# Optimization experiments

Measured on AMD Instinct MI355X. Metric: run time of the kernel, lower is better.

## Reference

```python
import jax, jax.numpy as jnp
import numpy as np

B, S, D, H, HD, TOPK = 2, 2048, 2048, 16, 128, 256
HIDDEN = 4 * D
EPS = 1e-6


def setup_inputs() -> dict:
    key = jax.random.key(0)
    ks = jax.random.split(key, 12)
    def g(k, shape, scale):
        return jax.random.normal(k, shape, dtype=jnp.float32) * scale
    # rotary tables: freqs_cis[s, i] = (cos, sin) of s * theta_i
    theta = 1.0 / (10000.0 ** (np.arange(0, HD, 2, dtype=np.float32) / HD))  # [HD/2]
    ang = np.arange(S, dtype=np.float32)[:, None] * theta[None, :]           # [S, HD/2]
    freqs_cis = jnp.asarray(np.stack([np.cos(ang), np.sin(ang)], axis=-1))   # [S, HD/2, 2]
    return {
        "x": g(ks[0], (B, S, D), 1.0),
        "start_pos": 0,
        "freqs_cis": freqs_cis,
        "router_w": g(ks[1], (D, 1), D ** -0.5),
        "wq": g(ks[2], (D, H * HD), D ** -0.5),
        "wk": g(ks[3], (D, H * HD), D ** -0.5),
        "wv": g(ks[4], (D, H * HD), D ** -0.5),
        "wo": g(ks[5], (H * HD, D), (H * HD) ** -0.5),
        "w1": g(ks[6], (D, HIDDEN), D ** -0.5),
        "w2": g(ks[7], (HIDDEN, D), HIDDEN ** -0.5),
        "w3": g(ks[8], (D, HIDDEN), D ** -0.5),
        "attn_norm_w": jnp.ones((D,), jnp.float32),
        "ffn_norm_w": jnp.ones((D,), jnp.float32),
    }


def _rmsnorm(x, w, eps=EPS):
    return x * jax.lax.rsqrt(jnp.mean(x * x, axis=-1, keepdims=True) + eps) * w


def _rotary(q, freqs):  # q: [B,S,H,HD], freqs: [S,HD/2,2]
    q = q.reshape(*q.shape[:-1], HD // 2, 2)
    cos = freqs[None, :, None, :, 0]
    sin = freqs[None, :, None, :, 1]
    qr = q[..., 0] * cos - q[..., 1] * sin
    qi = q[..., 0] * sin + q[..., 1] * cos
    return jnp.stack([qr, qi], axis=-1).reshape(*q.shape[:-2], HD)


def _attention(xn, freqs, tok_mask, wq, wk, wv, wo):
    b, s, _ = xn.shape
    q = (xn @ wq).reshape(b, s, H, HD)
    k = (xn @ wk).reshape(b, s, H, HD)
    v = (xn @ wv).reshape(b, s, H, HD)
    q = _rotary(q, freqs)
    k = _rotary(k, freqs)
    scores = jnp.einsum("bqhd,bkhd->bhqk", q, k) / np.sqrt(HD).astype(np.float32)
    # keys of non-selected tokens are masked out (MoD routing mask)
    scores = scores + jnp.where(tok_mask[:, None, None, :] > 0, 0.0, -1e9)
    attn = jax.nn.softmax(scores, axis=-1)
    out = jnp.einsum("bhqk,bkhd->bqhd", attn, v).reshape(b, s, H * HD)
    return out @ wo


def reference(x, start_pos, freqs_cis, router_w, wq, wk, wv, wo, w1, w2, w3, attn_norm_w, ffn_norm_w):
    b, s, _ = x.shape
    freqs = jax.lax.dynamic_slice_in_dim(freqs_cis, start_pos, s, axis=0)
    # --- router: top-k token selection + scatter mask ---
    token_weights = x @ router_w                      # [B,S,1]
    topk_vals, topk_idx = jax.lax.top_k(token_weights[..., 0], TOPK)
    mask = jnp.zeros((b, s), x.dtype).at[jnp.arange(b)[:, None], topk_idx].set(1.0)
    masked_input = x * mask[:, :, None]
    # --- dense attention + FFN on masked tokens ---
    h = masked_input + _attention(_rmsnorm(masked_input, attn_norm_w), freqs, mask, wq, wk, wv, wo)
    hn = _rmsnorm(h, ffn_norm_w)
    out = (jax.nn.silu(hn @ w1) * (hn @ w3)) @ w2    # SwiGLU FFN
    return out, token_weights, topk_idx
```

## Files before the change

kernel.cpp:

```cpp
#include <hip/hip_runtime.h>
#include <hip/hip_bf16.h>
#include <math.h>

#define B_ 2
#define S_ 2048
#define D_ 2048
#define H_ 16
#define HD_ 128
#define TOPK_ 256
#define HIDDEN_ 8192
#define EPS_ 1e-6f

constexpr int ROWS_SEL = B_ * TOPK_;
constexpr int ROWS_ALL = ROWS_SEL + B_;

typedef __attribute__((ext_vector_type(8))) short bf16x8;
typedef __attribute__((ext_vector_type(4))) float f32x4;

__device__ __forceinline__ short f2bf(float f) {
    __hip_bfloat16 h = __float2bfloat16(f);
    return *reinterpret_cast<short*>(&h);
}

__device__ __forceinline__ float bf2f(short s) {
    union { unsigned u; float f; } c;
    c.u = ((unsigned)(unsigned short)s) << 16;
    return c.f;
}

__device__ __forceinline__ void gll16(const void* g, void* l) {
    __builtin_amdgcn_global_load_lds(
        (const __attribute__((address_space(1))) unsigned int*)g,
        (__attribute__((address_space(3))) unsigned int*)l, 16, 0, 0);
}

__device__ __forceinline__ float block_sum_256(float v, float* red4) {
    for (int o = 32; o; o >>= 1) v += __shfl_down(v, o);
    if ((threadIdx.x & 63) == 0) red4[threadIdx.x >> 6] = v;
    __syncthreads();
    float t = red4[0] + red4[1] + red4[2] + red4[3];
    __syncthreads();
    return t;
}

__device__ __forceinline__ float block_max_256(float v, float* red4) {
    for (int o = 32; o; o >>= 1) v = fmaxf(v, __shfl_down(v, o));
    if ((threadIdx.x & 63) == 0) red4[threadIdx.x >> 6] = v;
    __syncthreads();
    float t = fmaxf(fmaxf(red4[0], red4[1]), fmaxf(red4[2], red4[3]));
    __syncthreads();
    return t;
}

__global__ __launch_bounds__(256) void router_kernel(const float* __restrict__ x,
                                                     const float* __restrict__ rw,
                                                     float* __restrict__ tw) {
    int token = blockIdx.x;
    const float4* xr = (const float4*)(x + (long)token * D_);
    const float4* r4 = (const float4*)rw;
    float s = 0.f;
    for (int c = threadIdx.x; c < D_ / 4; c += 256) {
        float4 a = xr[c], b = r4[c];
        s += a.x * b.x + a.y * b.y + a.z * b.z + a.w * b.w;
    }
    __shared__ float red4[4];
    float tot = block_sum_256(s, red4);
    if (threadIdx.x == 0) tw[token] = tot;
}

__global__ __launch_bounds__(1024) void topk_kernel(const float* __restrict__ tw,
                                                    float* __restrict__ idx_out,
                                                    int* __restrict__ sel_idx,
                                                    int* __restrict__ sel_pos) {
    int b = blockIdx.x;
    __shared__ float v[S_];
    __shared__ int id[S_];
    int t = threadIdx.x;
    for (int i = t; i < S_; i += 1024) {
        v[i] = tw[b * S_ + i];
        id[i] = i;
        sel_pos[b * S_ + i] = -1;
    }
    __syncthreads();
    for (int k = 2; k <= S_; k <<= 1) {
        for (int j = k >> 1; j > 0; j >>= 1) {
            for (int i = t; i < S_; i += 1024) {
                int ixj = i ^ j;
                if (ixj > i) {
                    float va = v[i], vb = v[ixj];
                    int ia = id[i], ib = id[ixj];
                    bool before = (va > vb) || (va == vb && ia < ib);
                    bool dir = ((i & k) == 0);
                    if (dir != before) {
                        v[i] = vb; v[ixj] = va;
                        id[i] = ib; id[ixj] = ia;
                    }
                }
            }
            __syncthreads();
        }
    }
    if (t < TOPK_) {
        idx_out[b * TOPK_ + t] = (float)id[t];
        sel_idx[b * TOPK_ + t] = id[t];
        sel_pos[b * S_ + id[t]] = t;
    }
}

__global__ __launch_bounds__(256) void gather_rmsnorm_kernel(const float* __restrict__ x,
                                                             const int* __restrict__ sel_idx,
                                                             const float* __restrict__ nw,
                                                             short* __restrict__ XN) {
    int r = blockIdx.x;
    int b = r >> 8;
    int s = sel_idx[r];
    const float* xr = x + ((long)b * S_ + s) * D_;
    __shared__ float buf[D_];
    __shared__ float red4[4];
    float ss = 0.f;
    for (int c = threadIdx.x; c < D_; c += 256) {
        float vv = xr[c];
        buf[c] = vv;
        ss += vv * vv;
    }
    float tot = block_sum_256(ss, red4);
    float scale = rsqrtf(tot / D_ + EPS_);
    for (int c = threadIdx.x; c < D_; c += 256)
        XN[(long)r * D_ + c] = f2bf(buf[c] * scale * nw[c]);
}

__global__ __launch_bounds__(256) void gemm_mfma_w(
    const short* __restrict__ A,
    const float* __restrict__ B0, const float* __restrict__ B1, const float* __restrict__ B2,
    float* __restrict__ Cb, long czStride, long spStride,
    int M, int N, int Ktot, int K_per, int splits) {
    __shared__ short As[128 * 32];
    __shared__ float Bs[32 * 128];
    int z = blockIdx.z;
    int zmat = z / splits, sp = z % splits;
    const float* Bm = (zmat == 0) ? B0 : (zmat == 1) ? B1 : B2;
    float* C = Cb + (long)zmat * czStride + (long)sp * spStride;
    int kbase = sp * K_per;
    int row0 = blockIdx.y * 128, col0 = blockIdx.x * 128;
    int t = threadIdx.x;
    int lane = t & 63, w = t >> 6;
    int l16 = lane & 15, quad = lane >> 4;
    int wr = (w >> 1) * 64, wc = (w & 1) * 64;
    int arr = t >> 2, ach = (t & 3) * 8;
    int bkr = t >> 5, bnc = (t & 31) * 4;
    f32x4 acc[4][4] = {};
    for (int k0 = kbase; k0 < kbase + K_per; k0 += 32) {
        __syncthreads();
        #pragma unroll
        for (int rd = 0; rd < 2; ++rd) {
            int ar = row0 + arr + rd * 64; ar = (ar < M) ? ar : (M - 1);
            gll16(A + (size_t)ar * Ktot + k0 + ach, (char*)As + rd * 4096 + t * 16);
        }
        #pragma unroll
        for (int rd = 0; rd < 4; ++rd) {
            int kr = k0 + rd * 8 + bkr;
            gll16(Bm + (size_t)kr * N + col0 + bnc, (char*)Bs + rd * 4096 + t * 16);
        }
        __syncthreads();
        bf16x8 af[4], bf[4];
        #pragma unroll
        for (int i = 0; i < 4; ++i)
            af[i] = *(const bf16x8*)(As + (wr + i * 16 + l16) * 32 + quad * 8);
        #pragma unroll
        for (int j = 0; j < 4; ++j) {
            int n = wc + j * 16 + l16;
            union { short s[8]; bf16x8 v; } ub;
            #pragma unroll
            for (int jj = 0; jj < 8; ++jj)
                ub.s[jj] = f2bf(Bs[(quad * 8 + jj) * 128 + n]);
            bf[j] = ub.v;
        }
        #pragma unroll
        for (int i = 0; i < 4; ++i)
            #pragma unroll
            for (int j = 0; j < 4; ++j)
                acc[i][j] = __builtin_amdgcn_mfma_f32_16x16x32_bf16(af[i], bf[j], acc[i][j], 0, 0, 0);
    }
    #pragma unroll
    for (int i = 0; i < 4; ++i) {
        #pragma unroll
        for (int r = 0; r < 4; ++r) {
            int row = row0 + wr + i * 16 + quad * 4 + r;
            if (row < M) {
                #pragma unroll
                for (int j = 0; j < 4; ++j)
                    C[(size_t)row * N + col0 + wc + j * 16 + l16] = acc[i][j][r];
            }
        }
    }
}

template <bool OBF>
__global__ __launch_bounds__(256) void gemm_mfma_attn(
    const short* __restrict__ A, long sAo, long sAi, int lda,
    const short* __restrict__ Bm, long sBo, long sBi, int ldb,
    void* __restrict__ Cv, long sCo, long sCi, int ldc,
    int M, int N, int K, int inner) {
    __shared__ short smem[2 * 128 * 32];
    short* As = smem;
    short* Bs = smem + 128 * 32;
    int z = blockIdx.z;
    int zo = z / inner, zi = z % inner;
    const short* Ab = A + (long)zo * sAo + (long)zi * sAi;
    const short* Bb = Bm + (long)zo * sBo + (long)zi * sBi;
    long cbase = (long)zo * sCo + (long)zi * sCi;
    int row0 = blockIdx.y * 128, col0 = blockIdx.x * 128;
    int t = threadIdx.x;
    int lane = t & 63, w = t >> 6;
    int l16 = lane & 15, quad = lane >> 4;
    int wr = (w >> 1) * 64, wc = (w & 1) * 64;
    int rr = t >> 2, ch = (t & 3) * 8;
    f32x4 acc[4][4] = {};
    for (int k0 = 0; k0 < K; k0 += 32) {
        __syncthreads();
        #pragma unroll
        for (int rd = 0; rd < 2; ++rd) {
            int r = rr + rd * 64;
            int ar = row0 + r; ar = (ar < M) ? ar : (M - 1);
            gll16(Ab + (size_t)ar * lda + k0 + ch, (char*)As + rd * 4096 + t * 16);
            gll16(Bb + (size_t)(col0 + r) * ldb + k0 + ch, (char*)Bs + rd * 4096 + t * 16);
        }
        __syncthreads();
        bf16x8 af[4], bfr[4];
        #pragma unroll
        for (int i = 0; i < 4; ++i)
            af[i] = *(const bf16x8*)(As + (wr + i * 16 + l16) * 32 + quad * 8);
        #pragma unroll
        for (int j = 0; j < 4; ++j)
            bfr[j] = *(const bf16x8*)(Bs + (wc + j * 16 + l16) * 32 + quad * 8);
        #pragma unroll
        for (int i = 0; i < 4; ++i)
            #pragma unroll
            for (int j = 0; j < 4; ++j)
                acc[i][j] = __builtin_amdgcn_mfma_f32_16x16x32_bf16(af[i], bfr[j], acc[i][j], 0, 0, 0);
    }
    #pragma unroll
    for (int i = 0; i < 4; ++i) {
        #pragma unroll
        for (int r = 0; r < 4; ++r) {
            int row = row0 + wr + i * 16 + quad * 4 + r;
            if (row < M) {
                #pragma unroll
                for (int j = 0; j < 4; ++j) {
                    long idx = cbase + (size_t)row * ldc + col0 + wc + j * 16 + l16;
                    if (OBF) ((short*)Cv)[idx] = f2bf(acc[i][j][r]);
                    else     ((float*)Cv)[idx] = acc[i][j][r];
                }
            }
        }
    }
}

__global__ __launch_bounds__(256) void qkv_finish(
    const float* __restrict__ Cp, const float* __restrict__ fc,
    const int* __restrict__ sel_idx, const int* __restrict__ sp0,
    short* __restrict__ Qbf, short* __restrict__ Kbf, short* __restrict__ Vbf,
    int splits) {
    int r = blockIdx.x;
    int s = sel_idx[r];
    int pos = sp0[0] + s;
    const float* f = fc + (long)pos * HD_;
    const long matS = (long)ROWS_SEL * D_;
    const long spS = 3 * matS;
    const float* qp = Cp + (long)r * D_;
    const float* kp = qp + matS;
    const float* vp = qp + 2 * matS;
    const float qscale = 0.08838834764831845f;
    for (int p = threadIdx.x; p < (D_ / 2); p += 256) {
        int h = p >> 6, d2 = p & 63;
        int e0 = h * HD_ + d2 * 2;
        float q0 = 0.f, q1 = 0.f, k0 = 0.f, k1 = 0.f, v0 = 0.f, v1 = 0.f;
        for (int sp = 0; sp < splits; ++sp) {
            long off = (long)sp * spS;
            q0 += qp[off + e0]; q1 += qp[off + e0 + 1];
            k0 += kp[off + e0]; k1 += kp[off + e0 + 1];
            v0 += vp[off + e0]; v1 += vp[off + e0 + 1];
        }
        float c = f[d2 * 2], sn = f[d2 * 2 + 1];
        Qbf[(long)r * D_ + e0]     = f2bf((q0 * c - q1 * sn) * qscale);
        Qbf[(long)r * D_ + e0 + 1] = f2bf((q0 * sn + q1 * c) * qscale);
        Kbf[(long)r * D_ + e0]     = f2bf(k0 * c - k1 * sn);
        Kbf[(long)r * D_ + e0 + 1] = f2bf(k0 * sn + k1 * c);
        Vbf[(long)r * D_ + e0]     = f2bf(v0);
        Vbf[(long)r * D_ + e0 + 1] = f2bf(v1);
    }
}

__global__ __launch_bounds__(256) void vt_kernel(const short* __restrict__ Vbf,
                                                 short* __restrict__ VT) {
    int z = blockIdx.z;
    int b = z >> 4, h = z & 15;
    int key0 = blockIdx.x * 64, d0 = blockIdx.y * 64;
    __shared__ short L[64][72];
    int t = threadIdx.x;
    int kr = t >> 3, dc = (t & 7) * 8;
    #pragma unroll
    for (int rr = 0; rr < 2; ++rr) {
        int key = kr + rr * 32;
        union { short s[8]; int4 v; } u;
        u.v = *(const int4*)&Vbf[(size_t)(b * 256 + key0 + key) * D_ + h * 128 + d0 + dc];
        #pragma unroll
        for (int j = 0; j < 8; ++j) L[key][dc + j] = u.s[j];
    }
    __syncthreads();
    int dr = t >> 3, kc = (t & 7) * 8;
    #pragma unroll
    for (int rr = 0; rr < 2; ++rr) {
        int d = dr + rr * 32;
        union { short s[8]; int4 v; } u;
        #pragma unroll
        for (int j = 0; j < 8; ++j) u.s[j] = L[kc + j][d];
        *(int4*)&VT[((size_t)z * 128 + d0 + d) * 256 + key0 + kc] = u.v;
    }
}

__global__ __launch_bounds__(256) void softmax_kernel(const float* __restrict__ SC,
                                                      short* __restrict__ Pbf) {
    long row = blockIdx.x;
    const float* p = SC + row * 256;
    int t = threadIdx.x;
    float v = p[t];
    __shared__ float red4[4];
    float m = block_max_256(v, red4);
    float e = expf(v - m);
    float s = block_sum_256(e, red4);
    Pbf[row * 256 + t] = f2bf(e / s);
}

__global__ __launch_bounds__(256) void vbar_kernel(const short* __restrict__ Vbf,
                                                   short* __restrict__ Obf) {
    int b = blockIdx.y;
    int c = blockIdx.x * 256 + threadIdx.x;
    float s = 0.f;
    for (int i = 0; i < TOPK_; ++i) s += bf2f(Vbf[((long)b * TOPK_ + i) * D_ + c]);
    Obf[(long)(ROWS_SEL + b) * D_ + c] = f2bf(s * (1.f / TOPK_));
}

__global__ __launch_bounds__(256) void resid_rmsnorm_kernel(const float* __restrict__ Pp,
                                                            int splits,
                                                            const float* __restrict__ x,
                                                            const int* __restrict__ sel_idx,
                                                            const float* __restrict__ nw,
                                                            short* __restrict__ HN) {
    int r = blockIdx.x;
    __shared__ float buf[D_];
    __shared__ float red4[4];
    const long spS = (long)ROWS_ALL * D_;
    const float* pr = Pp + (long)r * D_;
    const float* xr = nullptr;
    if (r < ROWS_SEL) {
        int b = r >> 8;
        int s = sel_idx[r];
        xr = x + ((long)b * S_ + s) * D_;
    }
    float ss = 0.f;
    for (int c = threadIdx.x; c < D_; c += 256) {
        float v = xr ? xr[c] : 0.f;
        for (int sp = 0; sp < splits; ++sp) v += pr[(long)sp * spS + c];
        buf[c] = v;
        ss += v * v;
    }
    float tot = block_sum_256(ss, red4);
    float scale = rsqrtf(tot / D_ + EPS_);
    for (int c = threadIdx.x; c < D_; c += 256)
        HN[(long)r * D_ + c] = f2bf(buf[c] * scale * nw[c]);
}

__global__ __launch_bounds__(256) void reduce_silu_kernel(const float* __restrict__ Gp,
                                                          short* __restrict__ FF, long n) {
    long i = (long)blockIdx.x * 256 + threadIdx.x;
    if (i < n) {
        const long cz = (long)ROWS_ALL * HIDDEN_;
        float a = Gp[i] + Gp[cz + i];
        float g = Gp[2 * cz + i] + Gp[3 * cz + i];
        FF[i] = f2bf((a / (1.f + expf(-a))) * g);
    }
}

__global__ __launch_bounds__(256) void w2_reduce_kernel(const float* __restrict__ Wp,
                                                        float* __restrict__ OUTR, long n4) {
    long i = (long)blockIdx.x * 256 + threadIdx.x;
    if (i < n4) {
        const long spS4 = (long)ROWS_ALL * D_ / 4;
        float4 s = ((const float4*)Wp)[i];
        for (int sp = 1; sp < 8; ++sp) {
            float4 v = ((const float4*)Wp)[(long)sp * spS4 + i];
            s.x += v.x; s.y += v.y; s.z += v.z; s.w += v.w;
        }
        ((float4*)OUTR)[i] = s;
    }
}

__global__ __launch_bounds__(256) void scatter_kernel(const float* __restrict__ OUTR,
                                                      const int* __restrict__ sel_pos,
                                                      float* __restrict__ out) {
    int blk = blockIdx.x;
    int b = blk >> 11;
    int p = sel_pos[blk];
    int row = (p >= 0) ? (b * TOPK_ + p) : (ROWS_SEL + b);
    const float4* src = (const float4*)(OUTR + (long)row * D_);
    float4* dst = (float4*)(out + (long)blk * D_);
    for (int c = threadIdx.x; c < D_ / 4; c += 256) dst[c] = src[c];
}

extern "C" void kernel_launch(void* const* d_in, const int* in_sizes, int n_in,
                              void* d_out, int out_size, void* d_ws, size_t ws_size,
                              hipStream_t stream) {
    const float* x        = (const float*)d_in[0];
    const int*   startpos = (const int*)d_in[1];
    const float* freqs    = (const float*)d_in[2];
    const float* router_w = (const float*)d_in[3];
    const float* wq       = (const float*)d_in[4];
    const float* wk       = (const float*)d_in[5];
    const float* wv       = (const float*)d_in[6];
    const float* wo       = (const float*)d_in[7];
    const float* w1       = (const float*)d_in[8];
    const float* w2       = (const float*)d_in[9];
    const float* w3       = (const float*)d_in[10];
    const float* attn_w   = (const float*)d_in[11];
    const float* ffn_w    = (const float*)d_in[12];

    float* out     = (float*)d_out;
    float* tw_out  = out + (long)B_ * S_ * D_;
    float* idx_out = tw_out + (long)B_ * S_;

    char* ws = (char*)d_ws;
    auto alloc = [&](size_t bytes) -> void* {
        void* p = (void*)ws;
        ws += (bytes + 255) / 256 * 256;
        return p;
    };
    int*   sel_idx = (int*)alloc((size_t)B_ * TOPK_ * sizeof(int));
    int*   sel_pos = (int*)alloc((size_t)B_ * S_ * sizeof(int));
    short* XNbf = (short*)alloc((size_t)ROWS_SEL * D_ * sizeof(short));
    short* Qbf  = (short*)alloc((size_t)ROWS_SEL * D_ * sizeof(short));
    short* Kbf  = (short*)alloc((size_t)ROWS_SEL * D_ * sizeof(short));
    short* Vbf  = (short*)alloc((size_t)ROWS_SEL * D_ * sizeof(short));
    short* VT   = (short*)alloc((size_t)B_ * H_ * HD_ * TOPK_ * sizeof(short));
    float* SC   = (float*)alloc((size_t)B_ * H_ * TOPK_ * TOPK_ * sizeof(float));
    short* Pbf  = (short*)alloc((size_t)B_ * H_ * TOPK_ * TOPK_ * sizeof(short));
    short* Obf  = (short*)alloc((size_t)ROWS_ALL * D_ * sizeof(short));
    short* HNbf = (short*)alloc((size_t)ROWS_ALL * D_ * sizeof(short));
    short* FFbf = (short*)alloc((size_t)ROWS_ALL * HIDDEN_ * sizeof(short));
    float* OUTR = (float*)alloc((size_t)ROWS_ALL * D_ * sizeof(float));
    float* Gar  = (float*)alloc((size_t)4 * ROWS_ALL * HIDDEN_ * sizeof(float));

    router_kernel<<<B_ * S_, 256, 0, stream>>>(x, router_w, tw_out);
    topk_kernel<<<B_, 1024, 0, stream>>>(tw_out, idx_out, sel_idx, sel_pos);
    gather_rmsnorm_kernel<<<ROWS_SEL, 256, 0, stream>>>(x, sel_idx, attn_w, XNbf);
    {
        dim3 g(D_ / 128, ROWS_SEL / 128, 3 * 4);
        gemm_mfma_w<<<g, 256, 0, stream>>>(XNbf, wq, wk, wv,
                                           Gar, (long)ROWS_SEL * D_, (long)3 * ROWS_SEL * D_,
                                           ROWS_SEL, D_, D_, D_ / 4, 4);
    }
    qkv_finish<<<ROWS_SEL, 256, 0, stream>>>(Gar, freqs, sel_idx, startpos, Qbf, Kbf, Vbf, 4);
    {
        dim3 g(4, 2, B_ * H_);
        vt_kernel<<<g, 256, 0, stream>>>(Vbf, VT);
    }
    {
        dim3 g(2, 2, B_ * H_);
        gemm_mfma_attn<false><<<g, 256, 0, stream>>>(
            Qbf, (long)TOPK_ * D_, HD_, D_,
            Kbf, (long)TOPK_ * D_, HD_, D_,
            SC, (long)H_ * TOPK_ * TOPK_, (long)TOPK_ * TOPK_, TOPK_,
            TOPK_, TOPK_, HD_, H_);
    }
    softmax_kernel<<<B_ * H_ * TOPK_, 256, 0, stream>>>(SC, Pbf);
    {
        dim3 g(1, 2, B_ * H_);
        gemm_mfma_attn<true><<<g, 256, 0, stream>>>(
            Pbf, (long)H_ * TOPK_ * TOPK_, (long)TOPK_ * TOPK_, TOPK_,
            VT, (long)H_ * HD_ * TOPK_, (long)HD_ * TOPK_, TOPK_,
            Obf, (long)TOPK_ * D_, HD_, D_,
            TOPK_, HD_, TOPK_, H_);
    }
    {
        dim3 g(D_ / 256, B_, 1);
        vbar_kernel<<<g, 256, 0, stream>>>(Vbf, Obf);
    }
    {
        dim3 g(D_ / 128, (ROWS_ALL + 127) / 128, 8);
        gemm_mfma_w<<<g, 256, 0, stream>>>(Obf, wo, wo, wo,
                                           Gar, 0, (long)ROWS_ALL * D_,
                                           ROWS_ALL, D_, D_, D_ / 8, 8);
    }
    resid_rmsnorm_kernel<<<ROWS_ALL, 256, 0, stream>>>(Gar, 8, x, sel_idx, ffn_w, HNbf);
    {
        dim3 g(HIDDEN_ / 128, (ROWS_ALL + 127) / 128, 2 * 2);
        gemm_mfma_w<<<g, 256, 0, stream>>>(HNbf, w1, w3, w3,
                                           Gar, (long)2 * ROWS_ALL * HIDDEN_, (long)ROWS_ALL * HIDDEN_,
                                           ROWS_ALL, HIDDEN_, D_, D_ / 2, 2);
    }
    {
        long n = (long)ROWS_ALL * HIDDEN_;
        reduce_silu_kernel<<<(unsigned)((n + 255) / 256), 256, 0, stream>>>(Gar, FFbf, n);
    }
    {
        dim3 g(D_ / 128, (ROWS_ALL + 127) / 128, 8);
        gemm_mfma_w<<<g, 256, 0, stream>>>(FFbf, w2, w2, w2,
                                           Gar, 0, (long)ROWS_ALL * D_,
                                           ROWS_ALL, D_, HIDDEN_, HIDDEN_ / 8, 8);
    }
    {
        long n4 = (long)ROWS_ALL * D_ / 4;
        w2_reduce_kernel<<<(unsigned)((n4 + 255) / 256), 256, 0, stream>>>(Gar, OUTR, n4);
    }
    scatter_kernel<<<B_ * S_, 256, 0, stream>>>(OUTR, sel_pos, out);
}
```

Before: 570.8 us.

## Pre-transpose weights to bf16 K-major and load B fragments directly

Adds a per-call kernel that converts each fp32 weight matrix to bf16 and transposes it to N×K layout through shared memory. The GEMM can then stage B tiles with the same 16-byte direct loads as A and read MFMA fragments as contiguous bf16x8 vectors. This removes the strided per-element fp32 LDS reads and bf16 conversions from the inner loop and halves LDS use for B. In exchange, every call makes an extra full pass over all weights: roughly 256MB read and 128MB written, plus extra workspace.

```diff
diff --git a/kernel.cpp b/kernel.cpp
--- a/kernel.cpp
+++ b/kernel.cpp
@@ -50,6 +50,34 @@
     float t = fmaxf(fmaxf(red4[0], red4[1]), fmaxf(red4[2], red4[3]));
     __syncthreads();
     return t;
+}
+
+__global__ __launch_bounds__(256) void wtrans_kernel(const float* __restrict__ Wsrc,
+                                                     short* __restrict__ WT,
+                                                     int K, int N) {
+    int k0 = blockIdx.y * 64, n0 = blockIdx.x * 64;
+    __shared__ short L[64][72];
+    int t = threadIdx.x;
+    int r = t >> 4, c4 = (t & 15) * 4;
+    #pragma unroll
+    for (int p = 0; p < 4; ++p) {
+        int kr = r + p * 16;
+        float4 v = *(const float4*)&Wsrc[(size_t)(k0 + kr) * N + n0 + c4];
+        L[kr][c4 + 0] = f2bf(v.x);
+        L[kr][c4 + 1] = f2bf(v.y);
+        L[kr][c4 + 2] = f2bf(v.z);
+        L[kr][c4 + 3] = f2bf(v.w);
+    }
+    __syncthreads();
+    int dr = t >> 3, kc = (t & 7) * 8;
+    #pragma unroll
+    for (int p = 0; p < 2; ++p) {
+        int n = dr + p * 32;
+        union { short s[8]; int4 v; } u;
+        #pragma unroll
+        for (int j = 0; j < 8; ++j) u.s[j] = L[kc + j][n];
+        *(int4*)&WT[(size_t)(n0 + n) * K + k0 + kc] = u.v;
+    }
 }
 
 __global__ __launch_bounds__(256) void router_kernel(const float* __restrict__ x,
@@ -129,16 +157,17 @@
         XN[(long)r * D_ + c] = f2bf(buf[c] * scale * nw[c]);
 }
 
-__global__ __launch_bounds__(256) void gemm_mfma_w(
+__global__ __launch_bounds__(256) void gemm_mfma_wbt(
     const short* __restrict__ A,
-    const float* __restrict__ B0, const float* __restrict__ B1, const float* __restrict__ B2,
+    const short* __restrict__ T0, const short* __restrict__ T1, const short* __restrict__ T2,
     float* __restrict__ Cb, long czStride, long spStride,
     int M, int N, int Ktot, int K_per, int splits) {
-    __shared__ short As[128 * 32];
-    __shared__ float Bs[32 * 128];
+    __shared__ short smem[2 * 128 * 32];
+    short* As = smem;
+    short* Bs = smem + 128 * 32;
     int z = blockIdx.z;
     int zmat = z / splits, sp = z % splits;
-    const float* Bm = (zmat == 0) ? B0 : (zmat == 1) ? B1 : B2;
+    const short* BT = (zmat == 0) ? T0 : (zmat == 1) ? T1 : T2;
     float* C = Cb + (long)zmat * czStride + (long)sp * spStride;
     int kbase = sp * K_per;
     int row0 = blockIdx.y * 128, col0 = blockIdx.x * 128;
@@ -146,40 +175,33 @@
     int lane = t & 63, w = t >> 6;
     int l16 = lane & 15, quad = lane >> 4;
     int wr = (w >> 1) * 64, wc = (w & 1) * 64;
-    int arr = t >> 2, ach = (t & 3) * 8;
-    int bkr = t >> 5, bnc = (t & 31) * 4;
+    int rr = t >> 2, ch = (t & 3) * 8;
+    int ar0 = row0 + rr;      ar0 = (ar0 < M) ? ar0 : (M - 1);
+    int ar1 = row0 + rr + 64; ar1 = (ar1 < M) ? ar1 : (M - 1);
+    const short* Ap0 = A + (size_t)ar0 * Ktot + ch;
+    const short* Ap1 = A + (size_t)ar1 * Ktot + ch;
+    const short* Bp0 = BT + (size_t)(col0 + rr) * Ktot + ch;
+    const short* Bp1 = BT + (size_t)(col0 + rr + 64) * Ktot + ch;
     f32x4 acc[4][4] = {};
     for (int k0 = kbase; k0 < kbase + K_per; k0 += 32) {
         __syncthreads();
-        #pragma unroll
-        for (int rd = 0; rd < 2; ++rd) {
-            int ar = row0 + arr + rd * 64; ar = (ar < M) ? ar : (M - 1);
-            gll16(A + (size_t)ar * Ktot + k0 + ach, (char*)As + rd * 4096 + t * 16);
-        }
-        #pragma unroll
-        for (int rd = 0; rd < 4; ++rd) {
-            int kr = k0 + rd * 8 + bkr;
-            gll16(Bm + (size_t)kr * N + col0 + bnc, (char*)Bs + rd * 4096 + t * 16);
-        }
+        gll16(Ap0 + k0, (char*)As + t * 16);
+        gll16(Ap1 + k0, (char*)As + 4096 + t * 16);
+        gll16(Bp0 + k0, (char*)Bs + t * 16);
+        gll16(Bp1 + k0, (char*)Bs + 4096 + t * 16);
         __syncthreads();
-        bf16x8 af[4], bf[4];
+        bf16x8 af[4], bfr[4];
         #pragma unroll
         for (int i = 0; i < 4; ++i)
             af[i] = *(const bf16x8*)(As + (wr + i * 16 + l16) * 32 + quad * 8);
         #pragma unroll
-        for (int j = 0; j < 4; ++j) {
-            int n = wc + j * 16 + l16;
-            union { short s[8]; bf16x8 v; } ub;
-            #pragma unroll
-            for (int jj = 0; jj < 8; ++jj)
-                ub.s[jj] = f2bf(Bs[(quad * 8 + jj) * 128 + n]);
-            bf[j] = ub.v;
-        }
+        for (int j = 0; j < 4; ++j)
+            bfr[j] = *(const bf16x8*)(Bs + (wc + j * 16 + l16) * 32 + quad * 8);
         #pragma unroll
         for (int i = 0; i < 4; ++i)
             #pragma unroll
             for (int j = 0; j < 4; ++j)
-                acc[i][j] = __builtin_amdgcn_mfma_f32_16x16x32_bf16(af[i], bf[j], acc[i][j], 0, 0, 0);
+                acc[i][j] = __builtin_amdgcn_mfma_f32_16x16x32_bf16(af[i], bfr[j], acc[i][j], 0, 0, 0);
     }
     #pragma unroll
     for (int i = 0; i < 4; ++i) {
@@ -448,16 +470,36 @@
     short* HNbf = (short*)alloc((size_t)ROWS_ALL * D_ * sizeof(short));
     short* FFbf = (short*)alloc((size_t)ROWS_ALL * HIDDEN_ * sizeof(short));
     float* OUTR = (float*)alloc((size_t)ROWS_ALL * D_ * sizeof(float));
+    short* wqT = (short*)alloc((size_t)D_ * D_ * sizeof(short));
+    short* wkT = (short*)alloc((size_t)D_ * D_ * sizeof(short));
+    short* wvT = (short*)alloc((size_t)D_ * D_ * sizeof(short));
+    short* woT = (short*)alloc((size_t)D_ * D_ * sizeof(short));
+    short* w1T = (short*)alloc((size_t)D_ * HIDDEN_ * sizeof(short));
+    short* w3T = (short*)alloc((size_t)D_ * HIDDEN_ * sizeof(short));
+    short* w2T = (short*)alloc((size_t)HIDDEN_ * D_ * sizeof(short));
     float* Gar  = (float*)alloc((size_t)4 * ROWS_ALL * HIDDEN_ * sizeof(float));
 
+    {
+        auto wt = [&](const float* src, short* dst, int K, int N) {
+            dim3 g(N / 64, K / 64);
+            wtrans_kernel<<<g, 256, 0, stream>>>(src, dst, K, N);
+        };
+        wt(wq, wqT, D_, D_);
+        wt(wk, wkT, D_, D_);
+        wt(wv, wvT, D_, D_);
+        wt(wo, woT, D_, D_);
+        wt(w1, w1T, D_, HIDDEN_);
+        wt(w3, w3T, D_, HIDDEN_);
+        wt(w2, w2T, HIDDEN_, D_);
+    }
     router_kernel<<<B_ * S_, 256, 0, stream>>>(x, router_w, tw_out);
     topk_kernel<<<B_, 1024, 0, stream>>>(tw_out, idx_out, sel_idx, sel_pos);
     gather_rmsnorm_kernel<<<ROWS_SEL, 256, 0, stream>>>(x, sel_idx, attn_w, XNbf);
     {
         dim3 g(D_ / 128, ROWS_SEL / 128, 3 * 4);
-        gemm_mfma_w<<<g, 256, 0, stream>>>(XNbf, wq, wk, wv,
-                                           Gar, (long)ROWS_SEL * D_, (long)3 * ROWS_SEL * D_,
-                                           ROWS_SEL, D_, D_, D_ / 4, 4);
+        gemm_mfma_wbt<<<g, 256, 0, stream>>>(XNbf, wqT, wkT, wvT,
+                                             Gar, (long)ROWS_SEL * D_, (long)3 * ROWS_SEL * D_,
+                                             ROWS_SEL, D_, D_, D_ / 4, 4);
     }
     qkv_finish<<<ROWS_SEL, 256, 0, stream>>>(Gar, freqs, sel_idx, startpos, Qbf, Kbf, Vbf, 4);
     {
@@ -487,16 +529,16 @@
     }
     {
         dim3 g(D_ / 128, (ROWS_ALL + 127) / 128, 8);
-        gemm_mfma_w<<<g, 256, 0, stream>>>(Obf, wo, wo, wo,
-                                           Gar, 0, (long)ROWS_ALL * D_,
-                                           ROWS_ALL, D_, D_, D_ / 8, 8);
+        gemm_mfma_wbt<<<g, 256, 0, stream>>>(Obf, woT, woT, woT,
+                                             Gar, 0, (long)ROWS_ALL * D_,
+                                             ROWS_ALL, D_, D_, D_ / 8, 8);
     }
     resid_rmsnorm_kernel<<<ROWS_ALL, 256, 0, stream>>>(Gar, 8, x, sel_idx, ffn_w, HNbf);
     {
         dim3 g(HIDDEN_ / 128, (ROWS_ALL + 127) / 128, 2 * 2);
-        gemm_mfma_w<<<g, 256, 0, stream>>>(HNbf, w1, w3, w3,
-                                           Gar, (long)2 * ROWS_ALL * HIDDEN_, (long)ROWS_ALL * HIDDEN_,
-                                           ROWS_ALL, HIDDEN_, D_, D_ / 2, 2);
+        gemm_mfma_wbt<<<g, 256, 0, stream>>>(HNbf, w1T, w3T, w3T,
+                                             Gar, (long)2 * ROWS_ALL * HIDDEN_, (long)ROWS_ALL * HIDDEN_,
+                                             ROWS_ALL, HIDDEN_, D_, D_ / 2, 2);
     }
     {
         long n = (long)ROWS_ALL * HIDDEN_;
@@ -504,9 +546,9 @@
     }
     {
         dim3 g(D_ / 128, (ROWS_ALL + 127) / 128, 8);
-        gemm_mfma_w<<<g, 256, 0, stream>>>(FFbf, w2, w2, w2,
-                                           Gar, 0, (long)ROWS_ALL * D_,
-                                           ROWS_ALL, D_, HIDDEN_, HIDDEN_ / 8, 8);
+        gemm_mfma_wbt<<<g, 256, 0, stream>>>(FFbf, w2T, w2T, w2T,
+                                             Gar, 0, (long)ROWS_ALL * D_,
+                                             ROWS_ALL, D_, HIDDEN_, HIDDEN_ / 8, 8);
     }
     {
         long n4 = (long)ROWS_ALL * D_ / 4;
```

Measured after the change: 617.9 us. 1.08x slower.
